# Kernel tuning notes

Hardware: AMD Instinct MI355X
Metric: run time of the kernel (lower is better)

The kernel has to match this reference:

```python
import jax, jax.numpy as jnp
import numpy as np

DIM = 24
HID = 256
N = 4096
NUM_LO = DIM * (DIM - 1) // 2  # 276
NEG = -0.01  # slope used in the hand-written Jacobians (source uses -0.01, NOT the fwd leaky slope 0.01; faithful)


def _linear_params(key, out_dim, in_dim):
    kw, kb = jax.random.split(key)
    s = 1.0 / np.sqrt(in_dim)
    W = jax.random.uniform(kw, (out_dim, in_dim), jnp.float32, -s, s)
    b = jax.random.uniform(kb, (out_dim,), jnp.float32, -s, s)
    return W, b


def setup_inputs() -> dict:
    key = jax.random.key(0)
    k = jax.random.split(key, 7)
    W1, b1 = _linear_params(k[0], HID, DIM)
    W2, b2 = _linear_params(k[1], HID, HID)
    WG, bG = _linear_params(k[2], DIM, HID)
    WLd, bLd = _linear_params(k[3], DIM, HID)
    WLo, bLo = _linear_params(k[4], NUM_LO, HID)
    q = jax.random.normal(k[5], (N, DIM), jnp.float32)
    q_dot = jax.random.normal(k[6], (N, DIM), jnp.float32)
    return {"q": q, "q_dot": q_dot, "W1": W1, "b1": b1, "W2": W2, "b2": b2,
            "WG": WG, "bG": bG, "WLd": WLd, "bLd": bLd, "WLo": WLo, "bLo": bLo}


def _forward(q, q_dot, W1, b1, W2, b2, WG, bG, WLd, bLd, WLo, bLo):
    n, d = q.shape
    tr, tc = np.tril_indices(d, -1)  # row-major strict-lower order == torch mask-flatten order
    di = np.arange(d)
    # MLP trunk (torch leaky_relu default slope 0.01)
    h1 = jax.nn.leaky_relu(q @ W1.T + b1)                       # [n,HID]
    h2 = jax.nn.leaky_relu(h1 @ W2.T + b2)                      # [n,HID]
    h3 = h2 @ WLd.T + bLd                                       # [n,d]
    g = h2 @ WG.T + bG                                          # [n,d]
    Ld = jax.nn.softplus(h3)                                    # [n,d]
    Lo = h2 @ WLo.T + bLo                                       # [n,NUM_LO]
    # Lower-triangular L (diag_embed(Ld) + masked strict-lower fill)
    L = jnp.zeros((n, d, d), q.dtype).at[:, tr, tc].set(Lo).at[:, di, di].set(Ld)
    # Hand-written Jacobian chain; diag_embed(v)@W == v[:,:,None]*W (direct elementwise scaling)
    dR1 = jnp.where(h1 > 0, 1.0, NEG)
    J1 = dR1[:, :, None] * W1                                    # dh1/dq  [n,HID,d]
    dR2 = jnp.where(h2 > 0, 1.0, NEG)
    J2 = dR2[:, :, None] * jnp.einsum('ij,njd->nid', W2, J1)     # dh2/dq  [n,HID,d]
    sig = jax.nn.sigmoid(h3)
    dld_dq = sig[:, :, None] * jnp.einsum('ij,njd->nid', WLd, J2)  # [n,d,d]
    dlo_dq = jnp.einsum('oj,njd->nod', WLo, J2)                  # [n,NUM_LO,d]
    dld_dt = jnp.einsum('nid,nd->ni', dld_dq, q_dot)             # [n,d]
    dlo_dt = jnp.einsum('nod,nd->no', dlo_dq, q_dot)             # [n,NUM_LO]
    dL_dt = jnp.zeros((n, d, d), q.dtype).at[:, tr, tc].set(dlo_dt).at[:, di, di].set(dld_dt)
    # 4D assembly: torch does L[L==1] = dlo_dq.view(-1), which reinterprets the (lo, q_idx)
    # flat buffer in (q_idx, tril_pos) order -> plain reshape replicates that exactly.
    vals = dlo_dq.reshape(n, d, NUM_LO)
    dld_dq_p = dld_dq.transpose(0, 2, 1)                         # [n, d_q, d_ld]
    dL_dq = jnp.zeros((n, d, d, d), q.dtype).at[:, :, tr, tc].set(vals).at[:, :, di, di].set(dld_dq_p)
    eye = jnp.eye(d, dtype=q.dtype)
    M = L @ L.transpose(0, 2, 1) + 1e-9 * eye
    dM_dt = L @ dL_dt.transpose(0, 2, 1) + dL_dt @ L.transpose(0, 2, 1)
    # Quadratic term. torch: q_dot.repeat(d,1)/L.repeat(d,1,1) index as (i % n) while
    # dL_dq.view(n*d,d,d) indexes as (i // d, i % d) -> replicate exactly (faithful).
    idx = jnp.arange(n * d) % n
    qd_r = q_dot[idx]                                            # [n*d, d]
    L_r = L[idx]                                                 # [n*d, d, d]
    dL_i = dL_dq.reshape(n * d, d, d)
    S = dL_i @ L_r.transpose(0, 2, 1) + L_r @ dL_i.transpose(0, 2, 1)
    quad = jnp.einsum('bi,bij,bj->b', qd_r, S, qd_r).reshape(n, d)
    c = jnp.einsum('nij,nj->ni', dM_dt, q_dot) - 0.5 * quad
    return M, c, g


def reference(q, q_dot, W1, b1, W2, b2, WG, bG, WLd, bLd, WLo, bLo):
    return _forward(q, q_dot, W1, b1, W2, b2, WG, bG, WLd, bLd, WLo, bLo)
```

## Files before the change

kernel.cpp:

```cpp
#include <hip/hip_runtime.h>
#include <math.h>

#define DIM 24
#define HID 256
#define NLO 276
#define NSAMP 4096
#define C_OFF 2359296
#define G_OFF 2457600

#define OFF_W2FH 0
#define OFF_W2FL 32768
#define OFF_WEFH 65536
#define OFF_WEFL 106496
#define OFF_W1H16 147456
#define OFF_W1L16 151552
#define OFF_W2H16 155648
#define OFF_W2L16 188416
#define OFF_WHH16 221184
#define OFF_WHL16 264192
#define OFF_MSKT 307200
#define OFF_SIGT 372736
#define OFF_LDT  471040
#define OFF_UT   569344
#define OFF_LOT  667648

typedef __attribute__((ext_vector_type(8))) short bf16x8;
typedef __attribute__((ext_vector_type(8))) _Float16 f16x8;
typedef __attribute__((ext_vector_type(4))) float f32x4;

__device__ __forceinline__ float leaky(float x){ return x > 0.f ? x : 0.01f*x; }
__device__ __forceinline__ unsigned short f2b(float f){
  unsigned u = __float_as_uint(f);
  return (unsigned short)((u + 0x7FFFu + ((u >> 16) & 1u)) >> 16);
}
__device__ __forceinline__ float b2f(unsigned short h){ return __uint_as_float(((unsigned)h) << 16); }
__device__ __forceinline__ void f2h2(float v, unsigned short* hi, unsigned short* lo){
  _Float16 h = (_Float16)v;
  _Float16 l = (_Float16)((v - (float)h) * 4096.f);
  *hi = *(unsigned short*)&h; *lo = *(unsigned short*)&l;
}

__global__ __launch_bounds__(256) void k0_prep(
    const float* __restrict__ W1, const float* __restrict__ W2,
    const float* __restrict__ WG, const float* __restrict__ WLd,
    const float* __restrict__ WLo, float* __restrict__ ws)
{
  const int tid = blockIdx.x*256 + threadIdx.x;
  const int nth = gridDim.x*256;
  unsigned short* W2FH = (unsigned short*)(ws + OFF_W2FH);
  unsigned short* W2FL = (unsigned short*)(ws + OFF_W2FL);
  for (int e = tid; e < 65536; e += nth){
    int j=e&7, l=(e>>3)&63, kb=(e>>9)&7, mt=e>>12;
    int m = mt*16+(l&15), k = kb*32+((l>>4)&3)*8+j;
    float v = W2[m*256+k];
    unsigned short h = f2b(v);
    W2FH[e]=h; W2FL[e]=f2b(v-b2f(h));
  }
  unsigned short* WEFH = (unsigned short*)(ws + OFF_WEFH);
  unsigned short* WEFL = (unsigned short*)(ws + OFF_WEFL);
  for (int e = tid; e < 81920; e += nth){
    int j=e&7, l=(e>>3)&63, kb=(e>>9)&7, mt=e>>12;
    int r = mt*16+(l&15), k = kb*32+((l>>4)&3)*8+j;
    float v = 0.f;
    if (r < 24) v = WLd[r*256+k]; else if (r < 300) v = WLo[(r-24)*256+k];
    unsigned short h = f2b(v);
    WEFH[e]=h; WEFL[e]=f2b(v-b2f(h));
  }
  unsigned short* W1H = (unsigned short*)(ws + OFF_W1H16);
  unsigned short* W1L = (unsigned short*)(ws + OFF_W1L16);
  for (int e = tid; e < 8192; e += nth){
    int j=e&7, l=(e>>3)&63, mt=e>>9;
    int m = mt*16+(l&15), k = ((l>>4)&3)*8+j;
    float v = (k < 24) ? W1[m*24+k] : 0.f;
    f2h2(v, &W1H[e], &W1L[e]);
  }
  unsigned short* W2H = (unsigned short*)(ws + OFF_W2H16);
  unsigned short* W2L = (unsigned short*)(ws + OFF_W2L16);
  for (int e = tid; e < 65536; e += nth){
    int j=e&7, l=(e>>3)&63, kb=(e>>9)&7, mt=e>>12;
    int m = mt*16+(l&15), k = kb*32+((l>>4)&3)*8+j;
    f2h2(W2[m*256+k], &W2H[e], &W2L[e]);
  }
  unsigned short* WHH = (unsigned short*)(ws + OFF_WHH16);
  unsigned short* WHL = (unsigned short*)(ws + OFF_WHL16);
  for (int e = tid; e < 86016; e += nth){
    int j=e&7, l=(e>>3)&63, kb=(e>>9)&7, mt=e>>12;
    int rr = mt*16+(l&15), k = kb*32+((l>>4)&3)*8+j;
    float v = 0.f;
    if (rr < 24) v = WLd[rr*256+k];
    else if (rr < 48) v = WG[(rr-24)*256+k];
    else if (rr < 324) v = WLo[(rr-48)*256+k];
    f2h2(v, &WHH[e], &WHL[e]);
  }
}

__global__ __launch_bounds__(256) void k1_fwd(
    const float* __restrict__ q, const float* __restrict__ qd_g,
    const float* __restrict__ b1, const float* __restrict__ b2,
    const float* __restrict__ bG, const float* __restrict__ bLd,
    const float* __restrict__ bLo, float* __restrict__ ws,
    float* __restrict__ out)
{
  const int s0 = blockIdx.x*32, t = threadIdx.x;
  const int w = t>>6, l = t&63, l15 = l&15, l4g = (l>>4)&3;
  unsigned* MSKT = (unsigned*)(ws + OFF_MSKT);
  float* SIGT = ws + OFF_SIGT;
  float* LDT  = ws + OFF_LDT;
  float* UT   = ws + OFF_UT;
  float* LOT  = ws + OFF_LOT;

  __shared__ __align__(16) char pool[33792];
  __shared__ float qd_s[32][24];
  __shared__ float Ld_s[32][24];
  __shared__ unsigned char mb[32][64];
  unsigned short* BQH = (unsigned short*)pool;
  unsigned short* BQL = BQH + 1280;
  unsigned short* BH2 = (unsigned short*)pool;
  unsigned short* BL2 = BH2 + 8448;

  for (int f = t; f < 768; f += 256){
    float v = q[s0*24 + f];
    int n = f/24, k = f%24;
    f2h2(v, &BQH[n*40+k], &BQL[n*40+k]);
    ((float*)qd_s)[f] = qd_g[s0*24 + f];
  }
  { int n = t>>3, k = 24 + (t&7); BQH[n*40+k]=0; BQL[n*40+k]=0; }
  __syncthreads();

  f32x4 aH[4][2], aX[4][2];
  #pragma unroll
  for (int i=0;i<4;++i) for (int nt=0;nt<2;++nt){ aH[i][nt]=(f32x4){0,0,0,0}; aX[i][nt]=(f32x4){0,0,0,0}; }
  {
    const f16x8* WH = (const f16x8*)(ws + OFF_W1H16);
    const f16x8* WL = (const f16x8*)(ws + OFF_W1L16);
    f16x8 Af[4], Al[4], Bh[2], Bl[2];
    #pragma unroll
    for (int i=0;i<4;++i){ int mt=w+4*i; Af[i]=WH[mt*64+l]; Al[i]=WL[mt*64+l]; }
    #pragma unroll
    for (int nt=0;nt<2;++nt){
      int off=(nt*16+l15)*40 + l4g*8;
      Bh[nt]=*(const f16x8*)(BQH+off); Bl[nt]=*(const f16x8*)(BQL+off);
    }
    #pragma unroll
    for (int i=0;i<4;++i)
      #pragma unroll
      for (int nt=0;nt<2;++nt){
        aH[i][nt]=__builtin_amdgcn_mfma_f32_16x16x32_f16(Af[i],Bh[nt],aH[i][nt],0,0,0);
        aX[i][nt]=__builtin_amdgcn_mfma_f32_16x16x32_f16(Af[i],Bl[nt],aX[i][nt],0,0,0);
        aX[i][nt]=__builtin_amdgcn_mfma_f32_16x16x32_f16(Al[i],Bh[nt],aX[i][nt],0,0,0);
      }
  }
  __syncthreads();
  #pragma unroll
  for (int i=0;i<4;++i){
    int m0=(w+4*i)*16+4*l4g;
    float4 bb = *(const float4*)(b1+m0);
    #pragma unroll
    for (int nt=0;nt<2;++nt){
      int n = nt*16+l15;
      unsigned nib=0; unsigned short hs[4], ls[4];
      #pragma unroll
      for (int r=0;r<4;++r){
        float val = aH[i][nt][r] + aX[i][nt][r]*(1.f/4096.f) + ((const float*)&bb)[r];
        if (val > 0.f) nib |= 1u<<r;
        f2h2(leaky(val), &hs[r], &ls[r]);
      }
      mb[n][(m0>>2)] = (unsigned char)nib;
      *(uint2*)(BH2 + n*264 + m0) = make_uint2((unsigned)hs[0]|((unsigned)hs[1]<<16),
                                               (unsigned)hs[2]|((unsigned)hs[3]<<16));
      *(uint2*)(BL2 + n*264 + m0) = make_uint2((unsigned)ls[0]|((unsigned)ls[1]<<16),
                                               (unsigned)ls[2]|((unsigned)ls[3]<<16));
    }
  }
  __syncthreads();
  {
    int n = t&31, w8 = t>>5; unsigned word = 0;
    #pragma unroll
    for (int b=0;b<8;++b) word |= (unsigned)(mb[n][w8*8+b] & 0xFu) << (4*b);
    MSKT[w8*NSAMP + s0+n] = word;
  }

  #pragma unroll
  for (int i=0;i<4;++i) for (int nt=0;nt<2;++nt){ aH[i][nt]=(f32x4){0,0,0,0}; aX[i][nt]=(f32x4){0,0,0,0}; }
  {
    const f16x8* WH = (const f16x8*)(ws + OFF_W2H16);
    const f16x8* WL = (const f16x8*)(ws + OFF_W2L16);
    for (int kb=0;kb<8;++kb){
      f16x8 Af[4], Al[4], Bh[2], Bl[2];
      #pragma unroll
      for (int i=0;i<4;++i){ int mt=w+4*i; Af[i]=WH[(mt*8+kb)*64+l]; Al[i]=WL[(mt*8+kb)*64+l]; }
      #pragma unroll
      for (int nt=0;nt<2;++nt){
        int off=(nt*16+l15)*264 + kb*32 + l4g*8;
        Bh[nt]=*(const f16x8*)(BH2+off); Bl[nt]=*(const f16x8*)(BL2+off);
      }
      #pragma unroll
      for (int i=0;i<4;++i)
        #pragma unroll
        for (int nt=0;nt<2;++nt){
          aH[i][nt]=__builtin_amdgcn_mfma_f32_16x16x32_f16(Af[i],Bh[nt],aH[i][nt],0,0,0);
          aX[i][nt]=__builtin_amdgcn_mfma_f32_16x16x32_f16(Af[i],Bl[nt],aX[i][nt],0,0,0);
          aX[i][nt]=__builtin_amdgcn_mfma_f32_16x16x32_f16(Al[i],Bh[nt],aX[i][nt],0,0,0);
        }
    }
  }
  __syncthreads();
  #pragma unroll
  for (int i=0;i<4;++i){
    int m0=(w+4*i)*16+4*l4g;
    float4 bb = *(const float4*)(b2+m0);
    #pragma unroll
    for (int nt=0;nt<2;++nt){
      int n = nt*16+l15;
      unsigned nib=0; unsigned short hs[4], ls[4];
      #pragma unroll
      for (int r=0;r<4;++r){
        float val = aH[i][nt][r] + aX[i][nt][r]*(1.f/4096.f) + ((const float*)&bb)[r];
        if (val > 0.f) nib |= 1u<<r;
        f2h2(leaky(val), &hs[r], &ls[r]);
      }
      mb[n][(m0>>2)] = (unsigned char)nib;
      *(uint2*)(BH2 + n*264 + m0) = make_uint2((unsigned)hs[0]|((unsigned)hs[1]<<16),
                                               (unsigned)hs[2]|((unsigned)hs[3]<<16));
      *(uint2*)(BL2 + n*264 + m0) = make_uint2((unsigned)ls[0]|((unsigned)ls[1]<<16),
                                               (unsigned)ls[2]|((unsigned)ls[3]<<16));
    }
  }
  __syncthreads();
  {
    int n = t&31, w8 = t>>5; unsigned word = 0;
    #pragma unroll
    for (int b=0;b<8;++b) word |= (unsigned)(mb[n][w8*8+b] & 0xFu) << (4*b);
    MSKT[(8+w8)*NSAMP + s0+n] = word;
  }

  for (int pass=0; pass<2; ++pass){
    f32x4 cH[3][2], cX[3][2];
    #pragma unroll
    for (int i=0;i<3;++i) for (int nt=0;nt<2;++nt){ cH[i][nt]=(f32x4){0,0,0,0}; cX[i][nt]=(f32x4){0,0,0,0}; }
    const f16x8* WH = (const f16x8*)(ws + OFF_WHH16);
    const f16x8* WL = (const f16x8*)(ws + OFF_WHL16);
    for (int kb=0;kb<8;++kb){
      f16x8 Af[3], Al[3], Bh[2], Bl[2];
      #pragma unroll
      for (int i=0;i<3;++i){
        int mt = w + 4*(3*pass+i);
        if (mt < 21){ Af[i]=WH[(mt*8+kb)*64+l]; Al[i]=WL[(mt*8+kb)*64+l]; }
      }
      #pragma unroll
      for (int nt=0;nt<2;++nt){
        int off=(nt*16+l15)*264 + kb*32 + l4g*8;
        Bh[nt]=*(const f16x8*)(BH2+off); Bl[nt]=*(const f16x8*)(BL2+off);
      }
      #pragma unroll
      for (int i=0;i<3;++i){
        int mt = w + 4*(3*pass+i);
        if (mt < 21){
          #pragma unroll
          for (int nt=0;nt<2;++nt){
            cH[i][nt]=__builtin_amdgcn_mfma_f32_16x16x32_f16(Af[i],Bh[nt],cH[i][nt],0,0,0);
            cX[i][nt]=__builtin_amdgcn_mfma_f32_16x16x32_f16(Af[i],Bl[nt],cX[i][nt],0,0,0);
            cX[i][nt]=__builtin_amdgcn_mfma_f32_16x16x32_f16(Al[i],Bh[nt],cX[i][nt],0,0,0);
          }
        }
      }
    }
    #pragma unroll
    for (int i=0;i<3;++i){
      int mt = w + 4*(3*pass+i);
      if (mt >= 21) continue;
      int m0 = mt*16+4*l4g;
      #pragma unroll
      for (int nt=0;nt<2;++nt){
        int n = nt*16+l15, sG = s0+n;
        #pragma unroll
        for (int r=0;r<4;++r){
          int rr = m0+r;
          float val = cH[i][nt][r] + cX[i][nt][r]*(1.f/4096.f);
          if (rr < 24){
            val += bLd[rr];
            SIGT[rr*NSAMP + sG] = 1.f/(1.f + expf(-val));
            float sp = fmaxf(val,0.f) + log1pf(expf(-fabsf(val)));
            LDT[rr*NSAMP + sG] = sp; Ld_s[n][rr] = sp;
          } else if (rr < 48){
            out[G_OFF + sG*24 + (rr-24)] = val + bG[rr-24];
          } else if (rr < 324){
            LOT[(rr-48)*NSAMP + sG] = val + bLo[rr-48];
          }
        }
      }
    }
  }
  __syncthreads();

  {
    int n = t&31, c = t>>5;
    for (; c < 24; c += 8){
      float u = qd_s[n][c]*Ld_s[n][c];
      for (int r=c+1; r<24; ++r) u += qd_s[n][r]*LOT[(r*(r-1)/2 + c)*NSAMP + s0+n];
      UT[c*NSAMP + s0+n] = u;
    }
  }
}

__global__ __launch_bounds__(256, 3) void kDE(
    const float* __restrict__ q_dot, const float* __restrict__ W1g,
    float* __restrict__ ws, float* __restrict__ out)
{
  const int n0 = blockIdx.x*2, t = threadIdx.x;
  const int w = t >> 6, l = t & 63;
  const int l15 = l & 15, l4g = (l >> 4) & 3;
  const unsigned* MSKT = (const unsigned*)(ws + OFF_MSKT);
  const float* SIGT = ws + OFF_SIGT;
  const float* LDT  = ws + OFF_LDT;
  const float* UT   = ws + OFF_UT;
  const float* LOT  = ws + OFF_LOT;

  __shared__ __align__(16) char pool[50688];
  __shared__ unsigned msk[2][16];
  unsigned short* BH = (unsigned short*)pool;
  unsigned short* BL = BH + 12672;
  float* Ef   = (float*)pool;
  float* Lp   = (float*)(pool + 30000);
  float* dtlo = (float*)(pool + 32400);
  float* dtld = (float*)(pool + 33504);
  float* w1s  = (float*)(pool + 33600);
  float* qps  = (float*)(pool + 33696);
  float* sigs = (float*)(pool + 34464);
  float* qds  = (float*)(pool + 34560);
  float* uss  = (float*)(pool + 34656);

  if (t < 32) msk[t>>4][t&15] = MSKT[(t&15)*NSAMP + n0 + (t>>4)];
  __syncthreads();

  {
    float w1r[24];
    #pragma unroll
    for (int d = 0; d < 24; ++d) w1r[d] = W1g[t*24 + d];
    float dr0 = ((msk[0][t>>5] >> (t&31)) & 1u) ? 1.f : -0.01f;
    float dr1 = ((msk[1][t>>5] >> (t&31)) & 1u) ? 1.f : -0.01f;
    #pragma unroll
    for (int c = 0; c < 48; ++c){
      int s = c >= 24, d = c - 24*s;
      float f = (s ? dr1 : dr0) * w1r[d];
      unsigned short h = f2b(f);
      BH[c*264 + t] = h;
      BL[c*264 + t] = f2b(f - b2f(h));
    }
  }
  __syncthreads();

  f32x4 accD[4][3];
  #pragma unroll
  for (int i = 0; i < 4; ++i)
    #pragma unroll
    for (int nt = 0; nt < 3; ++nt) accD[i][nt] = (f32x4){0.f,0.f,0.f,0.f};
  {
    const bf16x8* AHp = (const bf16x8*)(ws + OFF_W2FH);
    const bf16x8* ALp = (const bf16x8*)(ws + OFF_W2FL);
    for (int kb = 0; kb < 8; ++kb){
      bf16x8 AH[4], AL[4], BHf[3], BLf[3];
      #pragma unroll
      for (int i = 0; i < 4; ++i){
        int mt = 4*w + i;
        AH[i] = AHp[(mt*8+kb)*64 + l];
        AL[i] = ALp[(mt*8+kb)*64 + l];
      }
      #pragma unroll
      for (int nt = 0; nt < 3; ++nt){
        int off = (nt*16 + l15)*264 + kb*32 + l4g*8;
        BHf[nt] = *(const bf16x8*)(BH + off);
        BLf[nt] = *(const bf16x8*)(BL + off);
      }
      #pragma unroll
      for (int i = 0; i < 4; ++i)
        #pragma unroll
        for (int nt = 0; nt < 3; ++nt){
          accD[i][nt] = __builtin_amdgcn_mfma_f32_16x16x32_bf16(AH[i], BHf[nt], accD[i][nt], 0, 0, 0);
          accD[i][nt] = __builtin_amdgcn_mfma_f32_16x16x32_bf16(AH[i], BLf[nt], accD[i][nt], 0, 0, 0);
          accD[i][nt] = __builtin_amdgcn_mfma_f32_16x16x32_bf16(AL[i], BHf[nt], accD[i][nt], 0, 0, 0);
        }
    }
  }
  __syncthreads();

  #pragma unroll
  for (int i = 0; i < 4; ++i){
    int mt = 4*w + i;
    int m0 = mt*16 + 4*l4g;
    int bb = m0 & 31;
    #pragma unroll
    for (int nt = 0; nt < 3; ++nt){
      int c = nt*16 + l15;
      int s = c >= 24;
      unsigned word = msk[s][8 + (mt>>1)];
      unsigned short hs[4], ls[4];
      #pragma unroll
      for (int r = 0; r < 4; ++r){
        float sc = ((word >> (bb + r)) & 1u) ? 1.f : -0.01f;
        float v = sc * accD[i][nt][r];
        hs[r] = f2b(v); ls[r] = f2b(v - b2f(hs[r]));
      }
      *(uint2*)(BH + c*264 + m0) = make_uint2((unsigned)hs[0] | ((unsigned)hs[1]<<16),
                                              (unsigned)hs[2] | ((unsigned)hs[3]<<16));
      *(uint2*)(BL + c*264 + m0) = make_uint2((unsigned)ls[0] | ((unsigned)ls[1]<<16),
                                              (unsigned)ls[2] | ((unsigned)ls[3]<<16));
    }
  }
  __syncthreads();

  f32x4 accE[5][3];
  #pragma unroll
  for (int i = 0; i < 5; ++i)
    #pragma unroll
    for (int nt = 0; nt < 3; ++nt) accE[i][nt] = (f32x4){0.f,0.f,0.f,0.f};
  {
    const bf16x8* AHp = (const bf16x8*)(ws + OFF_WEFH);
    const bf16x8* ALp = (const bf16x8*)(ws + OFF_WEFL);
    for (int kb = 0; kb < 8; ++kb){
      bf16x8 AH[5], AL[5], BHf[3], BLf[3];
      #pragma unroll
      for (int i = 0; i < 5; ++i){
        int mt = 5*w + i;
        AH[i] = AHp[(mt*8+kb)*64 + l];
        AL[i] = ALp[(mt*8+kb)*64 + l];
      }
      #pragma unroll
      for (int nt = 0; nt < 3; ++nt){
        int off = (nt*16 + l15)*264 + kb*32 + l4g*8;
        BHf[nt] = *(const bf16x8*)(BH + off);
        BLf[nt] = *(const bf16x8*)(BL + off);
      }
      #pragma unroll
      for (int i = 0; i < 5; ++i)
        #pragma unroll
        for (int nt = 0; nt < 3; ++nt){
          accE[i][nt] = __builtin_amdgcn_mfma_f32_16x16x32_bf16(AH[i], BHf[nt], accE[i][nt], 0, 0, 0);
          accE[i][nt] = __builtin_amdgcn_mfma_f32_16x16x32_bf16(AH[i], BLf[nt], accE[i][nt], 0, 0, 0);
          accE[i][nt] = __builtin_amdgcn_mfma_f32_16x16x32_bf16(AL[i], BHf[nt], accE[i][nt], 0, 0, 0);
        }
    }
  }
  __syncthreads();

  for (int s = 0; s < 2; ++s){
    const int n = n0 + s;
    #pragma unroll
    for (int i = 0; i < 5; ++i){
      int mt = 5*w + i;
      #pragma unroll
      for (int nt = 0; nt < 3; ++nt){
        int c = nt*16 + l15;
        if ((c >= 24) == (s == 1)){
          int d = c - 24*s;
          #pragma unroll
          for (int r = 0; r < 4; ++r){
            int re = mt*16 + 4*l4g + r;
            if (re < 300) Ef[re*25 + d] = accE[i][nt][r];
          }
        }
      }
    }
    if (t < 24){
      sigs[t] = SIGT[t*NSAMP + n];
      qds[t]  = q_dot[n*24 + t];
      uss[t]  = UT[t*NSAMP + n];
      Lp[t*25 + t] = LDT[t*NSAMP + n];
    }
    for (int p = t; p < 276; p += 256){
      int r = (int)((1.f + sqrtf(1.f + 8.f*(float)p))*0.5f);
      while (r*(r-1)/2 > p) --r;
      while ((r+1)*r/2 <= p) ++r;
      int cc = p - r*(r-1)/2;
      Lp[r*25 + cc] = LOT[p*NSAMP + n];
    }
    __syncthreads();

    for (int e = t; e < 576; e += 256){
      int r = e/24, cc = e%24, km = min(r,cc);
      float acc = (r == cc) ? 1e-9f : 0.f;
      for (int k = 0; k <= km; ++k) acc += Lp[r*25+k]*Lp[cc*25+k];
      out[(size_t)n*576 + e] = acc;
    }
    for (int rr = t; rr < 300; rr += 256){
      float a = 0.f;
      #pragma unroll
      for (int d = 0; d < 24; ++d) a += Ef[rr*25 + d]*qds[d];
      if (rr < 24) dtld[rr] = sigs[rr]*a; else dtlo[rr-24] = a;
    }
    __syncthreads();

    if (t < 192){
      int i = t % 24, g = t / 24;
      int m = (n*24 + i) & (NSAMP-1);
      float qr[24];
      const float4* q4 = (const float4*)(q_dot + m*24);
      #pragma unroll
      for (int v4 = 0; v4 < 6; ++v4){
        float4 x = q4[v4];
        qr[4*v4+0]=x.x; qr[4*v4+1]=x.y; qr[4*v4+2]=x.z; qr[4*v4+3]=x.w;
      }
      float part = 0.f;
      for (int c2 = g; c2 < 24; c2 += 8){
        float v = qr[c2]*sigs[c2]*Ef[c2*25 + i];
        for (int r = c2+1; r < 24; ++r){
          int f = i*276 + r*(r-1)/2 + c2;
          v += qr[r]*Ef[(24 + f/24)*25 + (f%24)];
        }
        part += UT[c2*NSAMP + m]*v;
      }
      qps[g*24 + i] = part;
    } else if (t < 216){
      int i = t - 192;
      float a = qds[i]*dtld[i];
      for (int j = i+1; j < 24; ++j) a += qds[j]*dtlo[j*(j-1)/2 + i];
      w1s[i] = a;
    }
    __syncthreads();

    if (t < 24){
      int i = t;
      float cs = 0.f;
      for (int k = 0; k < i; ++k)
        cs += Lp[i*25+k]*w1s[k] + dtlo[i*(i-1)/2 + k]*uss[k];
      cs += Lp[i*25+i]*w1s[i] + dtld[i]*uss[i];
      float quad = 0.f;
      #pragma unroll
      for (int g = 0; g < 8; ++g) quad += qps[g*24 + i];
      out[C_OFF + n*24 + i] = cs - quad;
    }
    __syncthreads();
  }
}

extern "C" void kernel_launch(void* const* d_in, const int* in_sizes, int n_in,
                              void* d_out, int out_size, void* d_ws, size_t ws_size,
                              hipStream_t stream)
{
  const float* q   = (const float*)d_in[0];
  const float* qd  = (const float*)d_in[1];
  const float* W1  = (const float*)d_in[2];
  const float* b1  = (const float*)d_in[3];
  const float* W2  = (const float*)d_in[4];
  const float* b2  = (const float*)d_in[5];
  const float* WG  = (const float*)d_in[6];
  const float* bG  = (const float*)d_in[7];
  const float* WLd = (const float*)d_in[8];
  const float* bLd = (const float*)d_in[9];
  const float* WLo = (const float*)d_in[10];
  const float* bLo = (const float*)d_in[11];
  float* out = (float*)d_out;
  float* ws  = (float*)d_ws;

  k0_prep<<<256, 256, 0, stream>>>(W1, W2, WG, WLd, WLo, ws);
  k1_fwd<<<NSAMP/32, 256, 0, stream>>>(q, qd, b1, b2, bG, bLd, bLo, ws, out);
  kDE<<<NSAMP/2, 256, 0, stream>>>(qd, W1, ws, out);
}
```

Measured before the change: 288.3 us.

## Split forward into smaller blocks and move U and M computation into separate kernels

The forward kernel now processes 8 samples per block instead of 32, so more blocks are launched. Because only 8 of the 16 MFMA columns are used, half of each matrix-op's work is wasted. The U vector and the M = L·Lᵀ product move out of the forward and Jacobian kernels into two new kernels, kU and kM. The Jacobian kernel's quadratic term and dL/dt reduction are restructured with staged shared arrays and float4 reads. This shortens the serial tail of kDE and raises occupancy, at the cost of two extra launches and extra global traffic.

```diff
diff --git a/kernel.cpp b/kernel.cpp
--- a/kernel.cpp
+++ b/kernel.cpp
@@ -95,73 +95,63 @@
 }
 
 __global__ __launch_bounds__(256) void k1_fwd(
-    const float* __restrict__ q, const float* __restrict__ qd_g,
+    const float* __restrict__ q,
     const float* __restrict__ b1, const float* __restrict__ b2,
     const float* __restrict__ bG, const float* __restrict__ bLd,
     const float* __restrict__ bLo, float* __restrict__ ws,
     float* __restrict__ out)
 {
-  const int s0 = blockIdx.x*32, t = threadIdx.x;
+  const int s0 = blockIdx.x*8, t = threadIdx.x;
   const int w = t>>6, l = t&63, l15 = l&15, l4g = (l>>4)&3;
   unsigned* MSKT = (unsigned*)(ws + OFF_MSKT);
   float* SIGT = ws + OFF_SIGT;
   float* LDT  = ws + OFF_LDT;
-  float* UT   = ws + OFF_UT;
   float* LOT  = ws + OFF_LOT;
 
-  __shared__ __align__(16) char pool[33792];
-  __shared__ float qd_s[32][24];
-  __shared__ float Ld_s[32][24];
-  __shared__ unsigned char mb[32][64];
-  unsigned short* BQH = (unsigned short*)pool;
-  unsigned short* BQL = BQH + 1280;
-  unsigned short* BH2 = (unsigned short*)pool;
-  unsigned short* BL2 = BH2 + 8448;
-
-  for (int f = t; f < 768; f += 256){
+  __shared__ __align__(16) unsigned short pool[8448];
+  __shared__ unsigned char mb[8][64];
+  unsigned short* BQH = pool;
+  unsigned short* BQL = BQH + 320;
+  unsigned short* BH2 = pool;
+  unsigned short* BL2 = BH2 + 2112;
+
+  for (int f = t; f < 192; f += 256){
     float v = q[s0*24 + f];
     int n = f/24, k = f%24;
     f2h2(v, &BQH[n*40+k], &BQL[n*40+k]);
-    ((float*)qd_s)[f] = qd_g[s0*24 + f];
-  }
-  { int n = t>>3, k = 24 + (t&7); BQH[n*40+k]=0; BQL[n*40+k]=0; }
-  __syncthreads();
-
-  f32x4 aH[4][2], aX[4][2];
-  #pragma unroll
-  for (int i=0;i<4;++i) for (int nt=0;nt<2;++nt){ aH[i][nt]=(f32x4){0,0,0,0}; aX[i][nt]=(f32x4){0,0,0,0}; }
+  }
+  if (t < 64){ int n = t>>3, k = 24 + (t&7); BQH[n*40+k]=0; BQL[n*40+k]=0; }
+  __syncthreads();
+
+  f32x4 aH[4], aX[4];
+  #pragma unroll
+  for (int i=0;i<4;++i){ aH[i]=(f32x4){0,0,0,0}; aX[i]=(f32x4){0,0,0,0}; }
   {
     const f16x8* WH = (const f16x8*)(ws + OFF_W1H16);
     const f16x8* WL = (const f16x8*)(ws + OFF_W1L16);
-    f16x8 Af[4], Al[4], Bh[2], Bl[2];
+    f16x8 Af[4], Al[4];
     #pragma unroll
     for (int i=0;i<4;++i){ int mt=w+4*i; Af[i]=WH[mt*64+l]; Al[i]=WL[mt*64+l]; }
-    #pragma unroll
-    for (int nt=0;nt<2;++nt){
-      int off=(nt*16+l15)*40 + l4g*8;
-      Bh[nt]=*(const f16x8*)(BQH+off); Bl[nt]=*(const f16x8*)(BQL+off);
-    }
-    #pragma unroll
-    for (int i=0;i<4;++i)
-      #pragma unroll
-      for (int nt=0;nt<2;++nt){
-        aH[i][nt]=__builtin_amdgcn_mfma_f32_16x16x32_f16(Af[i],Bh[nt],aH[i][nt],0,0,0);
-        aX[i][nt]=__builtin_amdgcn_mfma_f32_16x16x32_f16(Af[i],Bl[nt],aX[i][nt],0,0,0);
-        aX[i][nt]=__builtin_amdgcn_mfma_f32_16x16x32_f16(Al[i],Bh[nt],aX[i][nt],0,0,0);
-      }
+    int off = l15*40 + l4g*8;
+    f16x8 Bh = *(const f16x8*)(BQH+off), Bl = *(const f16x8*)(BQL+off);
+    #pragma unroll
+    for (int i=0;i<4;++i){
+      aH[i]=__builtin_amdgcn_mfma_f32_16x16x32_f16(Af[i],Bh,aH[i],0,0,0);
+      aX[i]=__builtin_amdgcn_mfma_f32_16x16x32_f16(Af[i],Bl,aX[i],0,0,0);
+      aX[i]=__builtin_amdgcn_mfma_f32_16x16x32_f16(Al[i],Bh,aX[i],0,0,0);
+    }
   }
   __syncthreads();
   #pragma unroll
   for (int i=0;i<4;++i){
     int m0=(w+4*i)*16+4*l4g;
     float4 bb = *(const float4*)(b1+m0);
-    #pragma unroll
-    for (int nt=0;nt<2;++nt){
-      int n = nt*16+l15;
+    int n = l15;
+    if (n < 8){
       unsigned nib=0; unsigned short hs[4], ls[4];
       #pragma unroll
       for (int r=0;r<4;++r){
-        float val = aH[i][nt][r] + aX[i][nt][r]*(1.f/4096.f) + ((const float*)&bb)[r];
+        float val = aH[i][r] + aX[i][r]*(1.f/4096.f) + ((const float*)&bb)[r];
         if (val > 0.f) nib |= 1u<<r;
         f2h2(leaky(val), &hs[r], &ls[r]);
       }
@@ -173,35 +163,30 @@
     }
   }
   __syncthreads();
-  {
-    int n = t&31, w8 = t>>5; unsigned word = 0;
+  if (t < 64){
+    int n = t&7, w8 = t>>3; unsigned word = 0;
     #pragma unroll
     for (int b=0;b<8;++b) word |= (unsigned)(mb[n][w8*8+b] & 0xFu) << (4*b);
     MSKT[w8*NSAMP + s0+n] = word;
   }
 
   #pragma unroll
-  for (int i=0;i<4;++i) for (int nt=0;nt<2;++nt){ aH[i][nt]=(f32x4){0,0,0,0}; aX[i][nt]=(f32x4){0,0,0,0}; }
+  for (int i=0;i<4;++i){ aH[i]=(f32x4){0,0,0,0}; aX[i]=(f32x4){0,0,0,0}; }
   {
     const f16x8* WH = (const f16x8*)(ws + OFF_W2H16);
     const f16x8* WL = (const f16x8*)(ws + OFF_W2L16);
     for (int kb=0;kb<8;++kb){
-      f16x8 Af[4], Al[4], Bh[2], Bl[2];
+      f16x8 Af[4], Al[4];
       #pragma unroll
       for (int i=0;i<4;++i){ int mt=w+4*i; Af[i]=WH[(mt*8+kb)*64+l]; Al[i]=WL[(mt*8+kb)*64+l]; }
-      #pragma unroll
-      for (int nt=0;nt<2;++nt){
-        int off=(nt*16+l15)*264 + kb*32 + l4g*8;
-        Bh[nt]=*(const f16x8*)(BH2+off); Bl[nt]=*(const f16x8*)(BL2+off);
-      }
-      #pragma unroll
-      for (int i=0;i<4;++i)
-        #pragma unroll
-        for (int nt=0;nt<2;++nt){
-          aH[i][nt]=__builtin_amdgcn_mfma_f32_16x16x32_f16(Af[i],Bh[nt],aH[i][nt],0,0,0);
-          aX[i][nt]=__builtin_amdgcn_mfma_f32_16x16x32_f16(Af[i],Bl[nt],aX[i][nt],0,0,0);
-          aX[i][nt]=__builtin_amdgcn_mfma_f32_16x16x32_f16(Al[i],Bh[nt],aX[i][nt],0,0,0);
-        }
+      int off = l15*264 + kb*32 + l4g*8;
+      f16x8 Bh = *(const f16x8*)(BH2+off), Bl = *(const f16x8*)(BL2+off);
+      #pragma unroll
+      for (int i=0;i<4;++i){
+        aH[i]=__builtin_amdgcn_mfma_f32_16x16x32_f16(Af[i],Bh,aH[i],0,0,0);
+        aX[i]=__builtin_amdgcn_mfma_f32_16x16x32_f16(Af[i],Bl,aX[i],0,0,0);
+        aX[i]=__builtin_amdgcn_mfma_f32_16x16x32_f16(Al[i],Bh,aX[i],0,0,0);
+      }
     }
   }
   __syncthreads();
@@ -209,13 +194,12 @@
   for (int i=0;i<4;++i){
     int m0=(w+4*i)*16+4*l4g;
     float4 bb = *(const float4*)(b2+m0);
-    #pragma unroll
-    for (int nt=0;nt<2;++nt){
-      int n = nt*16+l15;
+    int n = l15;
+    if (n < 8){
       unsigned nib=0; unsigned short hs[4], ls[4];
       #pragma unroll
       for (int r=0;r<4;++r){
-        float val = aH[i][nt][r] + aX[i][nt][r]*(1.f/4096.f) + ((const float*)&bb)[r];
+        float val = aH[i][r] + aX[i][r]*(1.f/4096.f) + ((const float*)&bb)[r];
         if (val > 0.f) nib |= 1u<<r;
         f2h2(leaky(val), &hs[r], &ls[r]);
       }
@@ -227,41 +211,35 @@
     }
   }
   __syncthreads();
-  {
-    int n = t&31, w8 = t>>5; unsigned word = 0;
+  if (t < 64){
+    int n = t&7, w8 = t>>3; unsigned word = 0;
     #pragma unroll
     for (int b=0;b<8;++b) word |= (unsigned)(mb[n][w8*8+b] & 0xFu) << (4*b);
     MSKT[(8+w8)*NSAMP + s0+n] = word;
   }
 
   for (int pass=0; pass<2; ++pass){
-    f32x4 cH[3][2], cX[3][2];
-    #pragma unroll
-    for (int i=0;i<3;++i) for (int nt=0;nt<2;++nt){ cH[i][nt]=(f32x4){0,0,0,0}; cX[i][nt]=(f32x4){0,0,0,0}; }
+    f32x4 cH[3], cX[3];
+    #pragma unroll
+    for (int i=0;i<3;++i){ cH[i]=(f32x4){0,0,0,0}; cX[i]=(f32x4){0,0,0,0}; }
     const f16x8* WH = (const f16x8*)(ws + OFF_WHH16);
     const f16x8* WL = (const f16x8*)(ws + OFF_WHL16);
     for (int kb=0;kb<8;++kb){
-      f16x8 Af[3], Al[3], Bh[2], Bl[2];
+      f16x8 Af[3], Al[3];
       #pragma unroll
       for (int i=0;i<3;++i){
         int mt = w + 4*(3*pass+i);
         if (mt < 21){ Af[i]=WH[(mt*8+kb)*64+l]; Al[i]=WL[(mt*8+kb)*64+l]; }
       }
-      #pragma unroll
-      for (int nt=0;nt<2;++nt){
-        int off=(nt*16+l15)*264 + kb*32 + l4g*8;
-        Bh[nt]=*(const f16x8*)(BH2+off); Bl[nt]=*(const f16x8*)(BL2+off);
-      }
+      int off = l15*264 + kb*32 + l4g*8;
+      f16x8 Bh = *(const f16x8*)(BH2+off), Bl = *(const f16x8*)(BL2+off);
       #pragma unroll
       for (int i=0;i<3;++i){
         int mt = w + 4*(3*pass+i);
         if (mt < 21){
-          #pragma unroll
-          for (int nt=0;nt<2;++nt){
-            cH[i][nt]=__builtin_amdgcn_mfma_f32_16x16x32_f16(Af[i],Bh[nt],cH[i][nt],0,0,0);
-            cX[i][nt]=__builtin_amdgcn_mfma_f32_16x16x32_f16(Af[i],Bl[nt],cX[i][nt],0,0,0);
-            cX[i][nt]=__builtin_amdgcn_mfma_f32_16x16x32_f16(Al[i],Bh[nt],cX[i][nt],0,0,0);
-          }
+          cH[i]=__builtin_amdgcn_mfma_f32_16x16x32_f16(Af[i],Bh,cH[i],0,0,0);
+          cX[i]=__builtin_amdgcn_mfma_f32_16x16x32_f16(Af[i],Bl,cX[i],0,0,0);
+          cX[i]=__builtin_amdgcn_mfma_f32_16x16x32_f16(Al[i],Bh,cX[i],0,0,0);
         }
       }
     }
@@ -270,18 +248,17 @@
       int mt = w + 4*(3*pass+i);
       if (mt >= 21) continue;
       int m0 = mt*16+4*l4g;
-      #pragma unroll
-      for (int nt=0;nt<2;++nt){
-        int n = nt*16+l15, sG = s0+n;
+      int n = l15;
+      if (n < 8){
+        int sG = s0+n;
         #pragma unroll
         for (int r=0;r<4;++r){
           int rr = m0+r;
-          float val = cH[i][nt][r] + cX[i][nt][r]*(1.f/4096.f);
+          float val = cH[i][r] + cX[i][r]*(1.f/4096.f);
           if (rr < 24){
             val += bLd[rr];
             SIGT[rr*NSAMP + sG] = 1.f/(1.f + expf(-val));
-            float sp = fmaxf(val,0.f) + log1pf(expf(-fabsf(val)));
-            LDT[rr*NSAMP + sG] = sp; Ld_s[n][rr] = sp;
+            LDT[rr*NSAMP + sG] = fmaxf(val,0.f) + log1pf(expf(-fabsf(val)));
           } else if (rr < 48){
             out[G_OFF + sG*24 + (rr-24)] = val + bG[rr-24];
           } else if (rr < 324){
@@ -291,15 +268,54 @@
       }
     }
   }
-  __syncthreads();
-
-  {
-    int n = t&31, c = t>>5;
-    for (; c < 24; c += 8){
-      float u = qd_s[n][c]*Ld_s[n][c];
-      for (int r=c+1; r<24; ++r) u += qd_s[n][r]*LOT[(r*(r-1)/2 + c)*NSAMP + s0+n];
-      UT[c*NSAMP + s0+n] = u;
-    }
+}
+
+__global__ __launch_bounds__(256) void kU(
+    const float* __restrict__ qd_g, const float* __restrict__ ws_c,
+    float* __restrict__ UT)
+{
+  const int t = threadIdx.x, nb = blockIdx.x*256;
+  const float* LDT = ws_c + OFF_LDT;
+  const float* LOT = ws_c + OFF_LOT;
+  __shared__ float qd_ss[256*25];
+  for (int f = t; f < 6144; f += 256){
+    int nl = f/24, r = f%24;
+    qd_ss[nl*25 + r] = qd_g[nb*24 + f];
+  }
+  __syncthreads();
+  const int n = nb + t;
+  #pragma unroll
+  for (int c = 0; c < 24; ++c){
+    float u = qd_ss[t*25+c]*LDT[c*NSAMP + n];
+    for (int r = c+1; r < 24; ++r)
+      u += qd_ss[t*25+r]*LOT[(r*(r-1)/2 + c)*NSAMP + n];
+    UT[c*NSAMP + n] = u;
+  }
+}
+
+__global__ __launch_bounds__(256) void kM(
+    const float* __restrict__ ws_c, float* __restrict__ out)
+{
+  const int n = blockIdx.x, t = threadIdx.x;
+  const float* LDT = ws_c + OFF_LDT;
+  const float* LOT = ws_c + OFF_LOT;
+  __shared__ float Lp[600];
+  for (int e = t; e < 600; e += 256) Lp[e] = 0.f;
+  __syncthreads();
+  if (t < 24) Lp[t*25 + t] = LDT[t*NSAMP + n];
+  for (int p = t; p < 276; p += 256){
+    int r = (int)((1.f + sqrtf(1.f + 8.f*(float)p))*0.5f);
+    while (r*(r-1)/2 > p) --r;
+    while ((r+1)*r/2 <= p) ++r;
+    int c = p - r*(r-1)/2;
+    Lp[r*25 + c] = LOT[p*NSAMP + n];
+  }
+  __syncthreads();
+  for (int e = t; e < 576; e += 256){
+    int r = e/24, c = e%24, km = min(r,c);
+    float acc = (r == c) ? 1e-9f : 0.f;
+    for (int k = 0; k <= km; ++k) acc += Lp[r*25+k]*Lp[c*25+k];
+    out[(size_t)n*576 + e] = acc;
   }
 }
 
@@ -320,15 +336,17 @@
   __shared__ unsigned msk[2][16];
   unsigned short* BH = (unsigned short*)pool;
   unsigned short* BL = BH + 12672;
-  float* Ef   = (float*)pool;
-  float* Lp   = (float*)(pool + 30000);
-  float* dtlo = (float*)(pool + 32400);
-  float* dtld = (float*)(pool + 33504);
-  float* w1s  = (float*)(pool + 33600);
-  float* qps  = (float*)(pool + 33696);
-  float* sigs = (float*)(pool + 34464);
-  float* qds  = (float*)(pool + 34560);
-  float* uss  = (float*)(pool + 34656);
+  float* dlo_flat = (float*)pool;
+  float* dld25    = (float*)(pool + 26496);
+  float* qdm_s    = (float*)(pool + 28896);
+  float* um_s     = (float*)(pool + 31296);
+  float* qp2      = (float*)(pool + 33696);
+  float* dtlo     = (float*)(pool + 40320);
+  float* dtld     = (float*)(pool + 41424);
+  float* w1s      = (float*)(pool + 41520);
+  float* sigs     = (float*)(pool + 41616);
+  float* qds      = (float*)(pool + 41712);
+  float* uss      = (float*)(pool + 41808);
 
   if (t < 32) msk[t>>4][t&15] = MSKT[(t&15)*NSAMP + n0 + (t>>4)];
   __syncthreads();
@@ -456,62 +474,71 @@
           #pragma unroll
           for (int r = 0; r < 4; ++r){
             int re = mt*16 + 4*l4g + r;
-            if (re < 300) Ef[re*25 + d] = accE[i][nt][r];
+            if (re < 24) dld25[re*25 + d] = accE[i][nt][r];
+            else if (re < 300) dlo_flat[(re-24)*24 + d] = accE[i][nt][r];
           }
         }
       }
+    }
+    for (int e = t; e < 576; e += 256){
+      int a_ = e/24, b_ = e%24;
+      int ma = (n*24 + a_) & (NSAMP-1);
+      int mb_ = (n*24 + b_) & (NSAMP-1);
+      qdm_s[a_*25 + b_] = q_dot[ma*24 + b_];
+      um_s[a_*25 + b_]  = UT[a_*NSAMP + mb_];
     }
     if (t < 24){
       sigs[t] = SIGT[t*NSAMP + n];
       qds[t]  = q_dot[n*24 + t];
       uss[t]  = UT[t*NSAMP + n];
-      Lp[t*25 + t] = LDT[t*NSAMP + n];
-    }
-    for (int p = t; p < 276; p += 256){
-      int r = (int)((1.f + sqrtf(1.f + 8.f*(float)p))*0.5f);
-      while (r*(r-1)/2 > p) --r;
-      while ((r+1)*r/2 <= p) ++r;
-      int cc = p - r*(r-1)/2;
-      Lp[r*25 + cc] = LOT[p*NSAMP + n];
     }
     __syncthreads();
 
-    for (int e = t; e < 576; e += 256){
-      int r = e/24, cc = e%24, km = min(r,cc);
-      float acc = (r == cc) ? 1e-9f : 0.f;
-      for (int k = 0; k <= km; ++k) acc += Lp[r*25+k]*Lp[cc*25+k];
-      out[(size_t)n*576 + e] = acc;
-    }
-    for (int rr = t; rr < 300; rr += 256){
+    for (int k = t; k < 1656; k += 256){
+      float4 v = *(const float4*)(dlo_flat + 4*k);
+      int j4 = (k % 6)*4;
+      qp2[k] = v.x*qds[j4] + v.y*qds[j4+1] + v.z*qds[j4+2] + v.w*qds[j4+3];
+    }
+    if (t < 24){
       float a = 0.f;
       #pragma unroll
-      for (int d = 0; d < 24; ++d) a += Ef[rr*25 + d]*qds[d];
-      if (rr < 24) dtld[rr] = sigs[rr]*a; else dtlo[rr-24] = a;
+      for (int d = 0; d < 24; ++d) a += dld25[t*25+d]*qds[d];
+      dtld[t] = sigs[t]*a;
     }
     __syncthreads();
 
-    if (t < 192){
-      int i = t % 24, g = t / 24;
-      int m = (n*24 + i) & (NSAMP-1);
-      float qr[24];
-      const float4* q4 = (const float4*)(q_dot + m*24);
-      #pragma unroll
-      for (int v4 = 0; v4 < 6; ++v4){
-        float4 x = q4[v4];
-        qr[4*v4+0]=x.x; qr[4*v4+1]=x.y; qr[4*v4+2]=x.z; qr[4*v4+3]=x.w;
-      }
-      float part = 0.f;
-      for (int c2 = g; c2 < 24; c2 += 8){
-        float v = qr[c2]*sigs[c2]*Ef[c2*25 + i];
-        for (int r = c2+1; r < 24; ++r){
-          int f = i*276 + r*(r-1)/2 + c2;
-          v += qr[r]*Ef[(24 + f/24)*25 + (f%24)];
+    for (int o = t; o < 276; o += 256){
+      float a = 0.f;
+      #pragma unroll
+      for (int j = 0; j < 6; ++j) a += qp2[o*6+j];
+      dtlo[o] = a;
+    }
+    __syncthreads();
+
+    float quad_l = 0.f;
+    if (t < 24){
+      const int i = t;
+      float y[24];
+      #pragma unroll
+      for (int k = 0; k < 24; ++k) y[k] = um_s[k*25 + i];
+      #pragma unroll
+      for (int c2 = 0; c2 < 24; ++c2)
+        quad_l += y[c2]*qdm_s[i*25+c2]*sigs[c2]*dld25[c2*25+i];
+      const float* vb = dlo_flat + i*276;
+      float4 v4 = (float4){0,0,0,0};
+      #pragma unroll
+      for (int r = 1; r < 24; ++r){
+        float zr = qdm_s[i*25+r];
+        #pragma unroll
+        for (int cc = 0; cc < r; ++cc){
+          const int p = r*(r-1)/2 + cc;
+          if ((p & 3) == 0) v4 = *(const float4*)(vb + p);
+          float vbv = ((p&3)==0) ? v4.x : ((p&3)==1) ? v4.y : ((p&3)==2) ? v4.z : v4.w;
+          quad_l += zr*y[cc]*vbv;
         }
-        part += UT[c2*NSAMP + m]*v;
-      }
-      qps[g*24 + i] = part;
-    } else if (t < 216){
-      int i = t - 192;
+      }
+    } else if (t >= 64 && t < 88){
+      int i = t - 64;
       float a = qds[i]*dtld[i];
       for (int j = i+1; j < 24; ++j) a += qds[j]*dtlo[j*(j-1)/2 + i];
       w1s[i] = a;
@@ -519,15 +546,13 @@
     __syncthreads();
 
     if (t < 24){
-      int i = t;
-      float cs = 0.f;
-      for (int k = 0; k < i; ++k)
-        cs += Lp[i*25+k]*w1s[k] + dtlo[i*(i-1)/2 + k]*uss[k];
-      cs += Lp[i*25+i]*w1s[i] + dtld[i]*uss[i];
-      float quad = 0.f;
-      #pragma unroll
-      for (int g = 0; g < 8; ++g) quad += qps[g*24 + i];
-      out[C_OFF + n*24 + i] = cs - quad;
+      const int i = t;
+      float cs = dtld[i]*uss[i] + LDT[i*NSAMP + n]*w1s[i];
+      for (int k = 0; k < i; ++k){
+        int p = i*(i-1)/2 + k;
+        cs += LOT[p*NSAMP + n]*w1s[k] + dtlo[p]*uss[k];
+      }
+      out[C_OFF + n*24 + i] = cs - quad_l;
     }
     __syncthreads();
   }
@@ -553,6 +578,8 @@
   float* ws  = (float*)d_ws;
 
   k0_prep<<<256, 256, 0, stream>>>(W1, W2, WG, WLd, WLo, ws);
-  k1_fwd<<<NSAMP/32, 256, 0, stream>>>(q, qd, b1, b2, bG, bLd, bLo, ws, out);
+  k1_fwd<<<NSAMP/8, 256, 0, stream>>>(q, b1, b2, bG, bLd, bLo, ws, out);
+  kU<<<NSAMP/256, 256, 0, stream>>>(qd, ws, ws + OFF_UT);
+  kM<<<NSAMP, 256, 0, stream>>>(ws, out);
   kDE<<<NSAMP/2, 256, 0, stream>>>(qd, W1, ws, out);
 }
```

New measurement: 266.3 us. 7.6% less time.
